# Performance work log

Measured on AMD Instinct MI355X. Metric: run time of the kernel, lower is better.

The kernel has to match this reference:

```python
import jax, jax.numpy as jnp
import numpy as np

N = 100000      # num nodes
E = 1600000     # num edges (avg degree 16)
IN = 128        # in_channels
OUT = 64        # out_channels
HID = 2 * OUT   # conv1 output width = 2*out_channels


def setup_inputs() -> dict:
    key = jax.random.key(0)
    k0, k1, k2, k3 = jax.random.split(key, 4)
    x = jax.random.uniform(k0, (N, IN), dtype=jnp.float32)
    edge_index = jax.random.randint(k1, (2, E), 0, N, dtype=jnp.int32)
    # GCNConv weights (glorot-style uniform), biases zero-init as in PyG
    s1 = float(np.sqrt(6.0 / (IN + HID)))
    W1 = jax.random.uniform(k2, (IN, HID), minval=-s1, maxval=s1, dtype=jnp.float32)
    b1 = jnp.zeros((HID,), dtype=jnp.float32)
    s2 = float(np.sqrt(6.0 / (HID + OUT)))
    W2 = jax.random.uniform(k3, (HID, OUT), minval=-s2, maxval=s2, dtype=jnp.float32)
    b2 = jnp.zeros((OUT,), dtype=jnp.float32)
    return {"x": x, "edge_index": edge_index, "W1": W1, "b1": b1, "W2": W2, "b2": b2}


def gcn_conv(x, W, b, src, dst, n):
    """PyG GCNConv: self-loops + symmetric deg^-1/2 normalization + scatter-add."""
    h = x @ W                                   # [n, d_out] dense transform first
    loops = jnp.arange(n, dtype=src.dtype)
    s = jnp.concatenate([src, loops])           # [E+n] sources (with self-loops)
    d = jnp.concatenate([dst, loops])           # [E+n] destinations
    deg = jax.ops.segment_sum(jnp.ones_like(s, dtype=h.dtype), d, num_segments=n)
    dinv = jnp.where(deg > 0, jax.lax.rsqrt(deg), 0.0)
    norm = dinv[s] * dinv[d]                    # [E+n]
    # gather -> scale -> scatter-add aggregation
    out = jax.ops.segment_sum(h[s] * norm[:, None], d, num_segments=n)
    return out + b


def reference(x, edge_index, W1, b1, W2, b2):
    src, dst = edge_index[0], edge_index[1]
    n = x.shape[0]
    h = jax.nn.relu(gcn_conv(x, W1, b1, src, dst, n))
    return gcn_conv(h, W2, b2, src, dst, n)
```

## Files before the change

### kernel.cpp

```cpp
#include <hip/hip_runtime.h>

#define IN_C  128
#define HID_C 128
#define OUT_C 64
#define NPB      128
#define NPB_SH   7
#define NPB_MASK 127
#define MAXB     2048
#define CAP      8192
#define B1_CHUNK 4096
#define PADQ     16
#define PADSLACK ((PADQ - 1) * NPB)

typedef __attribute__((ext_vector_type(8))) short short8;
typedef __attribute__((ext_vector_type(4))) float f32x4;

__device__ __forceinline__ unsigned short f2bf(float f) {
    unsigned u = __float_as_uint(f);
    unsigned r = (u + 0x7FFFu + ((u >> 16) & 1u)) >> 16;
    return (unsigned short)r;
}
__device__ __forceinline__ float bf_lo(unsigned u) { return __uint_as_float(u << 16); }
__device__ __forceinline__ float bf_hi(unsigned u) { return __uint_as_float(u & 0xFFFF0000u); }


__global__ __launch_bounds__(256) void hist_kernel(const int* __restrict__ dst,
                                                   int* __restrict__ bhist,
                                                   int E, int B) {
    __shared__ int lh[MAXB];
    int t = threadIdx.x;
    int e0 = blockIdx.x * B1_CHUNK;
    int nE = min(B1_CHUNK, E - e0);
    if (B <= MAXB) {
        for (int i = t; i < B; i += 256) lh[i] = 0;
        __syncthreads();
        for (int i = t; i < nE; i += 256) atomicAdd(&lh[dst[e0 + i] >> NPB_SH], 1);
        __syncthreads();
        for (int i = t; i < B; i += 256)
            if (lh[i]) atomicAdd(&bhist[i], lh[i]);
    } else {
        for (int i = t; i < nE; i += 256) atomicAdd(&bhist[dst[e0 + i] >> NPB_SH], 1);
    }
}

__global__ __launch_bounds__(1024) void scan_bucket_kernel(const int* __restrict__ bhist,
                                                           int* __restrict__ bbase,
                                                           int* __restrict__ bcur, int B) {
    __shared__ int sums[1024];
    int t = threadIdx.x;
    int chunk = (B + 1023) >> 10;
    int beg = t * chunk, end = min(beg + chunk, B);
    int s = 0;
    for (int i = beg; i < end; ++i) s += bhist[i];
    sums[t] = s;
    __syncthreads();
    for (int off = 1; off < 1024; off <<= 1) {
        int v = (t >= off) ? sums[t - off] : 0;
        __syncthreads();
        sums[t] += v;
        __syncthreads();
    }
    int run = (t == 0) ? 0 : sums[t - 1];
    for (int i = beg; i < end; ++i) {
        bbase[i] = run;
        bcur[i] = run + i * PADSLACK;
        run += bhist[i];
    }
    if (t == 1023) bbase[B] = sums[1023];
}

__global__ __launch_bounds__(256) void bucket_kernel(const int* __restrict__ src,
                                                     const int* __restrict__ dst,
                                                     int* __restrict__ bcur,
                                                     int* __restrict__ col,
                                                     int E, int B) {
    __shared__ int hist[MAXB];
    __shared__ int runb[MAXB];
    int t = threadIdx.x;
    int e0 = blockIdx.x * B1_CHUNK;
    int nE = min(B1_CHUNK, E - e0);
    if (B <= MAXB) {
        for (int i = t; i < B; i += 256) hist[i] = 0;
        __syncthreads();
        for (int i = t; i < nE; i += 256) atomicAdd(&hist[dst[e0 + i] >> NPB_SH], 1);
        __syncthreads();
        for (int i = t; i < B; i += 256) {
            int c = hist[i];
            runb[i] = c ? atomicAdd(&bcur[i], c) : 0;
            hist[i] = 0;
        }
        __syncthreads();
        for (int i = t; i < nE; i += 256) {
            int d = dst[e0 + i], s = src[e0 + i];
            int b = d >> NPB_SH;
            int off2 = atomicAdd(&hist[b], 1);
            col[runb[b] + off2] = (s << NPB_SH) | (d & NPB_MASK);
        }
    } else {
        for (int i = t; i < nE; i += 256) {
            int d = dst[e0 + i], s = src[e0 + i];
            int pos = atomicAdd(&bcur[d >> NPB_SH], 1);
            col[pos] = (s << NPB_SH) | (d & NPB_MASK);
        }
    }
}

__global__ __launch_bounds__(256) void csr_kernel(int* __restrict__ col,
                                                  const int* __restrict__ bbase,
                                                  int* __restrict__ rowptr,
                                                  int* __restrict__ rowend,
                                                  float* __restrict__ dinv,
                                                  int N, int E) {
    __shared__ int sorted[CAP];
    __shared__ int lhist[NPB];
    __shared__ int lpre[NPB + 1];
    int b = blockIdx.x;
    int t = threadIdx.x;
    int size = bbase[b + 1] - bbase[b];
    int pbase = bbase[b] + b * PADSLACK;
    int node_base = b << NPB_SH;
    int nn = min(NPB, N - node_base);

    if (t < NPB) lhist[t] = 0;
    __syncthreads();
    for (int i = t; i < size; i += 256) atomicAdd(&lhist[col[pbase + i] & NPB_MASK], 1);
    __syncthreads();
    if (t < NPB) lpre[t + 1] = (lhist[t] + PADQ - 1) & ~(PADQ - 1);
    if (t == 0) lpre[0] = 0;
    __syncthreads();
    for (int off = 1; off < NPB; off <<= 1) {
        int v = (t >= off && t < NPB) ? lpre[t + 1 - off] : 0;
        __syncthreads();
        if (t < NPB) lpre[t + 1] += v;
        __syncthreads();
    }
    if (t < nn) {
        rowptr[node_base + t] = pbase + lpre[t];
        rowend[node_base + t] = pbase + lpre[t + 1];
        dinv[node_base + t] = rsqrtf((float)(lhist[t] + 1));
    }
    if (t < NPB) lhist[t] = lpre[t];
    __syncthreads();
    int psize = lpre[NPB];
    if (psize <= CAP) {
        for (int i = t; i < psize; i += 256) sorted[i] = N;
        __syncthreads();
        for (int i = t; i < size; i += 256) {
            int entry = col[pbase + i];
            int slot = atomicAdd(&lhist[entry & NPB_MASK], 1);
            sorted[slot] = entry >> NPB_SH;
        }
        __syncthreads();
        for (int i = t; i < psize; i += 256) col[pbase + i] = sorted[i];
    } else {
        int ent[32];
        int c2 = 0;
        for (int i = t; i < size && c2 < 32; i += 256) ent[c2++] = col[pbase + i];
        __syncthreads();
        for (int i = t; i < psize; i += 256) col[pbase + i] = N;
        __syncthreads();
        c2 = 0;
        for (int i = t; i < size && c2 < 32; i += 256) {
            int entry = ent[c2++];
            int slot = atomicAdd(&lhist[entry & NPB_MASK], 1);
            col[pbase + slot] = entry >> NPB_SH;
        }
    }
}


template<int C, typename InT>
__global__ __launch_bounds__(256) void mm_mfma_kernel(
    const InT* __restrict__ X, const float* __restrict__ W,
    const float* __restrict__ dinv, unsigned short* __restrict__ Hs, int n) {
    constexpr int LD = 136;
    __shared__ unsigned short Wt[C][LD];
    int t = threadIdx.x;

    if (blockIdx.x == 0) {
        for (int i = t; i < C / 2; i += 256)
            ((unsigned*)(Hs + (size_t)n * C))[i] = 0;
    }

    for (int i = t; i < (128 * C) / 4; i += 256) {
        int idx = i * 4;
        int k = idx / C, c = idx % C;
        float4 wv = *(const float4*)&W[(size_t)k * C + c];
        Wt[c + 0][k] = f2bf(wv.x);
        Wt[c + 1][k] = f2bf(wv.y);
        Wt[c + 2][k] = f2bf(wv.z);
        Wt[c + 3][k] = f2bf(wv.w);
    }
    __syncthreads();

    int w = t >> 6, lane = t & 63;
    int m = lane & 15, quad = lane >> 4;
    int row0 = blockIdx.x * 64 + w * 16;
    int arow = min(row0 + m, n - 1);

    constexpr int NT = C / 16;
    f32x4 acc[NT];
#pragma unroll
    for (int ct = 0; ct < NT; ++ct) acc[ct] = (f32x4){0.f, 0.f, 0.f, 0.f};

#pragma unroll
    for (int kk = 0; kk < 4; ++kk) {
        int k0 = kk * 32 + quad * 8;
        short8 a;
        if constexpr (sizeof(InT) == 4) {
            const float* xp = (const float*)X + (size_t)arow * 128 + k0;
            float4 f0 = *(const float4*)xp;
            float4 f1 = *(const float4*)(xp + 4);
            a[0] = (short)f2bf(f0.x); a[1] = (short)f2bf(f0.y);
            a[2] = (short)f2bf(f0.z); a[3] = (short)f2bf(f0.w);
            a[4] = (short)f2bf(f1.x); a[5] = (short)f2bf(f1.y);
            a[6] = (short)f2bf(f1.z); a[7] = (short)f2bf(f1.w);
        } else {
            a = *(const short8*)((const unsigned short*)X + (size_t)arow * 128 + k0);
        }
#pragma unroll
        for (int ct = 0; ct < NT; ++ct) {
            short8 b = *(const short8*)&Wt[ct * 16 + m][k0];
            acc[ct] = __builtin_amdgcn_mfma_f32_16x16x32_bf16(a, b, acc[ct], 0, 0, 0);
        }
    }

    int qrow = row0 + quad * 4;
    float dv[4];
#pragma unroll
    for (int r = 0; r < 4; ++r) dv[r] = (qrow + r < n) ? dinv[qrow + r] : 0.f;
#pragma unroll
    for (int ct = 0; ct < NT; ++ct) {
        int c = ct * 16 + m;
#pragma unroll
        for (int r = 0; r < 4; ++r) {
            int row = qrow + r;
            if (row < n) Hs[(size_t)row * C + c] = f2bf(acc[ct][r] * dv[r]);
        }
    }
}


#define GBODY(NB)                                                              \
    {                                                                          \
        uint4 v[NB];                                                           \
        _Pragma("unroll") for (int b = 0; b < NB; ++b) {                       \
            int e = (g + b) * SLOTS + slot;                                    \
            int idx = __shfl(colv, e, 64);                                     \
            v[b] = *((const uint4*)(Hs + (size_t)idx * C) + cl);               \
        }                                                                      \
        _Pragma("unroll") for (int b = 0; b < NB; ++b) {                       \
            acc[0] += bf_lo(v[b].x); acc[1] += bf_hi(v[b].x);                  \
            acc[2] += bf_lo(v[b].y); acc[3] += bf_hi(v[b].y);                  \
            acc[4] += bf_lo(v[b].z); acc[5] += bf_hi(v[b].z);                  \
            acc[6] += bf_lo(v[b].w); acc[7] += bf_hi(v[b].w);                  \
        }                                                                      \
    }

template<int C, bool BOUT>
__global__ __launch_bounds__(256) void agg_kernel(
    const unsigned short* __restrict__ Hs, const float* __restrict__ bias,
    const float* __restrict__ dinv, const int* __restrict__ rowptr,
    const int* __restrict__ rowend, const int* __restrict__ col,
    void* __restrict__ outv, int n, int relu) {
    constexpr int LPR = C / 8;
    constexpr int SLOTS = 64 / LPR;
    int d = (blockIdx.x * 256 + threadIdx.x) >> 6;
    if (d >= n) return;
    int lane = threadIdx.x & 63;
    int cl = lane & (LPR - 1);
    int slot = lane / LPR;

    float acc[8] = {0.f, 0.f, 0.f, 0.f, 0.f, 0.f, 0.f, 0.f};
    int beg = rowptr[d], end = rowend[d];

    for (int j0 = beg; j0 < end; j0 += 64) {
        int cnt = min(64, end - j0);
        int colv = col[j0 + lane];
        int groups = cnt / SLOTS;
        int g = 0;
        for (; g + 4 <= groups; g += 4) GBODY(4)
        if constexpr (SLOTS == 8) {
            if (g < groups) GBODY(2)
        }
    }
#pragma unroll
    for (int mk = LPR; mk < 64; mk <<= 1) {
#pragma unroll
        for (int k = 0; k < 8; ++k) acc[k] += __shfl_xor(acc[k], mk, 64);
    }
    uint4 sv = *((const uint4*)(Hs + (size_t)d * C) + cl);
    acc[0] += bf_lo(sv.x); acc[1] += bf_hi(sv.x);
    acc[2] += bf_lo(sv.y); acc[3] += bf_hi(sv.y);
    acc[4] += bf_lo(sv.z); acc[5] += bf_hi(sv.z);
    acc[6] += bf_lo(sv.w); acc[7] += bf_hi(sv.w);

    float dv = dinv[d];
    float4 b0 = *((const float4*)bias + cl * 2);
    float4 b1 = *((const float4*)bias + cl * 2 + 1);
    float r[8];
    r[0] = dv * acc[0] + b0.x; r[1] = dv * acc[1] + b0.y;
    r[2] = dv * acc[2] + b0.z; r[3] = dv * acc[3] + b0.w;
    r[4] = dv * acc[4] + b1.x; r[5] = dv * acc[5] + b1.y;
    r[6] = dv * acc[6] + b1.z; r[7] = dv * acc[7] + b1.w;
    if (relu) {
#pragma unroll
        for (int k = 0; k < 8; ++k) r[k] = fmaxf(r[k], 0.f);
    }
    if (slot == 0) {
        if constexpr (BOUT) {
            uint4 o;
            o.x = (unsigned)f2bf(r[0]) | ((unsigned)f2bf(r[1]) << 16);
            o.y = (unsigned)f2bf(r[2]) | ((unsigned)f2bf(r[3]) << 16);
            o.z = (unsigned)f2bf(r[4]) | ((unsigned)f2bf(r[5]) << 16);
            o.w = (unsigned)f2bf(r[6]) | ((unsigned)f2bf(r[7]) << 16);
            *(uint4*)((unsigned short*)outv + (size_t)d * C + cl * 8) = o;
        } else {
            float* o = (float*)outv + (size_t)d * C + cl * 8;
            *(float4*)o = make_float4(r[0], r[1], r[2], r[3]);
            *(float4*)(o + 4) = make_float4(r[4], r[5], r[6], r[7]);
        }
    }
}


extern "C" void kernel_launch(void* const* d_in, const int* in_sizes, int n_in,
                              void* d_out, int out_size, void* d_ws, size_t ws_size,
                              hipStream_t stream) {
    const float* x  = (const float*)d_in[0];
    const int*   ei = (const int*)d_in[1];
    const float* W1 = (const float*)d_in[2];
    const float* b1 = (const float*)d_in[3];
    const float* W2 = (const float*)d_in[4];
    const float* b2 = (const float*)d_in[5];
    float* out = (float*)d_out;

    int N = in_sizes[0] / IN_C;
    int E = in_sizes[1] / 2;
    const int* src = ei;
    const int* dst = ei + E;
    int B = (N + NPB - 1) >> NPB_SH;
    int nblk = (E + B1_CHUNK - 1) / B1_CHUNK;

    char* ws = (char*)d_ws;
    size_t off = 0;
    int*   bhist  = (int*)(ws + off);   off += (size_t)B * 4;
    int*   bbase  = (int*)(ws + off);   off += (size_t)(B + 1) * 4;
    int*   bcur   = (int*)(ws + off);   off += (size_t)B * 4;
    float* dinv   = (float*)(ws + off); off += (size_t)N * 4;
    int*   rowptr = (int*)(ws + off);   off += (size_t)N * 4;
    int*   rowend = (int*)(ws + off);   off += (size_t)N * 4;
    off = (off + 15) & ~(size_t)15;
    int*   col    = (int*)(ws + off);   off += ((size_t)E + (size_t)B * PADSLACK + 64) * 4;
    off = (off + 15) & ~(size_t)15;
    unsigned short* H1  = (unsigned short*)(ws + off); off += (size_t)(N + 1) * HID_C * 2;
    off = (off + 15) & ~(size_t)15;
    unsigned short* AG1 = (unsigned short*)(ws + off); off += (size_t)N * HID_C * 2;
    unsigned short* H2 = H1;

    hipMemsetAsync(bhist, 0, (size_t)B * 4, stream);

    hist_kernel<<<nblk, 256, 0, stream>>>(dst, bhist, E, B);
    scan_bucket_kernel<<<1, 1024, 0, stream>>>(bhist, bbase, bcur, B);
    bucket_kernel<<<nblk, 256, 0, stream>>>(src, dst, bcur, col, E, B);
    csr_kernel<<<B, 256, 0, stream>>>(col, bbase, rowptr, rowend, dinv, N, E);

    int mblk = (N + 63) / 64;
    mm_mfma_kernel<HID_C, float><<<mblk, 256, 0, stream>>>(x, W1, dinv, H1, N);
    agg_kernel<HID_C, true><<<(N + 3) / 4, 256, 0, stream>>>(
        H1, b1, dinv, rowptr, rowend, col, AG1, N, 1);

    mm_mfma_kernel<OUT_C, unsigned short><<<mblk, 256, 0, stream>>>(AG1, W2, dinv, H2, N);
    agg_kernel<OUT_C, false><<<(N + 3) / 4, 256, 0, stream>>>(
        H2, b2, dinv, rowptr, rowend, col, out, N, 0);
}
```

Before: 347.3 us.

## Process multiple destination nodes per wavefront in aggregation kernels

The aggregation kernel now assigns NPN destination rows to each 64-lane wavefront (2 for the 128-wide layer, 4 for the 64-wide layer) and interleaves their neighbor gathers, so more independent loads are in flight per wave. Column indices are fetched with nontemporal loads. This aims to raise memory-level parallelism and amortize per-row setup, but costs more registers, idles lanes when neighboring rows have very different degrees, and launches fewer waves overall.

```diff
diff --git a/kernel.cpp b/kernel.cpp
--- a/kernel.cpp
+++ b/kernel.cpp
@@ -241,23 +241,7 @@
 }
 
 
-#define GBODY(NB)                                                              \
-    {                                                                          \
-        uint4 v[NB];                                                           \
-        _Pragma("unroll") for (int b = 0; b < NB; ++b) {                       \
-            int e = (g + b) * SLOTS + slot;                                    \
-            int idx = __shfl(colv, e, 64);                                     \
-            v[b] = *((const uint4*)(Hs + (size_t)idx * C) + cl);               \
-        }                                                                      \
-        _Pragma("unroll") for (int b = 0; b < NB; ++b) {                       \
-            acc[0] += bf_lo(v[b].x); acc[1] += bf_hi(v[b].x);                  \
-            acc[2] += bf_lo(v[b].y); acc[3] += bf_hi(v[b].y);                  \
-            acc[4] += bf_lo(v[b].z); acc[5] += bf_hi(v[b].z);                  \
-            acc[6] += bf_lo(v[b].w); acc[7] += bf_hi(v[b].w);                  \
-        }                                                                      \
-    }
-
-template<int C, bool BOUT>
+template<int C, bool BOUT, int NPN>
 __global__ __launch_bounds__(256) void agg_kernel(
     const unsigned short* __restrict__ Hs, const float* __restrict__ bias,
     const float* __restrict__ dinv, const int* __restrict__ rowptr,
@@ -265,60 +249,116 @@
     void* __restrict__ outv, int n, int relu) {
     constexpr int LPR = C / 8;
     constexpr int SLOTS = 64 / LPR;
-    int d = (blockIdx.x * 256 + threadIdx.x) >> 6;
-    if (d >= n) return;
+    constexpr int U = (SLOTS == 4) ? 4 : 2;
+    int wid = (blockIdx.x * 256 + threadIdx.x) >> 6;
+    int d0 = wid * NPN;
+    if (d0 >= n) return;
     int lane = threadIdx.x & 63;
     int cl = lane & (LPR - 1);
     int slot = lane / LPR;
 
-    float acc[8] = {0.f, 0.f, 0.f, 0.f, 0.f, 0.f, 0.f, 0.f};
-    int beg = rowptr[d], end = rowend[d];
-
-    for (int j0 = beg; j0 < end; j0 += 64) {
-        int cnt = min(64, end - j0);
-        int colv = col[j0 + lane];
-        int groups = cnt / SLOTS;
-        int g = 0;
-        for (; g + 4 <= groups; g += 4) GBODY(4)
-        if constexpr (SLOTS == 8) {
-            if (g < groups) GBODY(2)
-        }
-    }
-#pragma unroll
-    for (int mk = LPR; mk < 64; mk <<= 1) {
-#pragma unroll
-        for (int k = 0; k < 8; ++k) acc[k] += __shfl_xor(acc[k], mk, 64);
-    }
-    uint4 sv = *((const uint4*)(Hs + (size_t)d * C) + cl);
-    acc[0] += bf_lo(sv.x); acc[1] += bf_hi(sv.x);
-    acc[2] += bf_lo(sv.y); acc[3] += bf_hi(sv.y);
-    acc[4] += bf_lo(sv.z); acc[5] += bf_hi(sv.z);
-    acc[6] += bf_lo(sv.w); acc[7] += bf_hi(sv.w);
-
-    float dv = dinv[d];
+    int beg[NPN], len[NPN];
+    float dv[NPN];
+    uint4 sv[NPN];
+#pragma unroll
+    for (int k = 0; k < NPN; ++k) {
+        int d = d0 + k;
+        int dd = min(d, n - 1);
+        beg[k] = rowptr[dd];
+        len[k] = (d < n) ? (rowend[dd] - beg[k]) : 0;
+        dv[k] = dinv[dd];
+        sv[k] = *((const uint4*)(Hs + (size_t)dd * C) + cl);
+    }
+
+    float acc[NPN][8];
+#pragma unroll
+    for (int k = 0; k < NPN; ++k)
+#pragma unroll
+        for (int q = 0; q < 8; ++q) acc[k][q] = 0.f;
+
+    int lmax = 0;
+#pragma unroll
+    for (int k = 0; k < NPN; ++k) lmax = max(lmax, len[k]);
+
+    for (int j0 = 0; j0 < lmax; j0 += 64) {
+        int colv[NPN], groups[NPN];
+#pragma unroll
+        for (int k = 0; k < NPN; ++k)
+            colv[k] = __builtin_nontemporal_load(col + beg[k] + j0 + lane);
+#pragma unroll
+        for (int k = 0; k < NPN; ++k) {
+            int c = len[k] - j0;
+            c = c < 0 ? 0 : (c > 64 ? 64 : c);
+            groups[k] = c / SLOTS;
+        }
+        int gmax = 0;
+#pragma unroll
+        for (int k = 0; k < NPN; ++k) gmax = max(gmax, groups[k]);
+        for (int g = 0; g < gmax; g += U) {
+            uint4 v[NPN][U];
+#pragma unroll
+            for (int k = 0; k < NPN; ++k) {
+                if (g < groups[k]) {
+#pragma unroll
+                    for (int b = 0; b < U; ++b) {
+                        int e = (g + b) * SLOTS + slot;
+                        int idx = __shfl(colv[k], e, 64);
+                        v[k][b] = *((const uint4*)(Hs + (size_t)idx * C) + cl);
+                    }
+                }
+            }
+#pragma unroll
+            for (int k = 0; k < NPN; ++k) {
+                if (g < groups[k]) {
+#pragma unroll
+                    for (int b = 0; b < U; ++b) {
+                        acc[k][0] += bf_lo(v[k][b].x); acc[k][1] += bf_hi(v[k][b].x);
+                        acc[k][2] += bf_lo(v[k][b].y); acc[k][3] += bf_hi(v[k][b].y);
+                        acc[k][4] += bf_lo(v[k][b].z); acc[k][5] += bf_hi(v[k][b].z);
+                        acc[k][6] += bf_lo(v[k][b].w); acc[k][7] += bf_hi(v[k][b].w);
+                    }
+                }
+            }
+        }
+    }
+
     float4 b0 = *((const float4*)bias + cl * 2);
     float4 b1 = *((const float4*)bias + cl * 2 + 1);
-    float r[8];
-    r[0] = dv * acc[0] + b0.x; r[1] = dv * acc[1] + b0.y;
-    r[2] = dv * acc[2] + b0.z; r[3] = dv * acc[3] + b0.w;
-    r[4] = dv * acc[4] + b1.x; r[5] = dv * acc[5] + b1.y;
-    r[6] = dv * acc[6] + b1.z; r[7] = dv * acc[7] + b1.w;
-    if (relu) {
-#pragma unroll
-        for (int k = 0; k < 8; ++k) r[k] = fmaxf(r[k], 0.f);
-    }
-    if (slot == 0) {
-        if constexpr (BOUT) {
-            uint4 o;
-            o.x = (unsigned)f2bf(r[0]) | ((unsigned)f2bf(r[1]) << 16);
-            o.y = (unsigned)f2bf(r[2]) | ((unsigned)f2bf(r[3]) << 16);
-            o.z = (unsigned)f2bf(r[4]) | ((unsigned)f2bf(r[5]) << 16);
-            o.w = (unsigned)f2bf(r[6]) | ((unsigned)f2bf(r[7]) << 16);
-            *(uint4*)((unsigned short*)outv + (size_t)d * C + cl * 8) = o;
-        } else {
-            float* o = (float*)outv + (size_t)d * C + cl * 8;
-            *(float4*)o = make_float4(r[0], r[1], r[2], r[3]);
-            *(float4*)(o + 4) = make_float4(r[4], r[5], r[6], r[7]);
+#pragma unroll
+    for (int k = 0; k < NPN; ++k) {
+        int d = d0 + k;
+        if (d >= n) break;
+#pragma unroll
+        for (int mk = LPR; mk < 64; mk <<= 1) {
+#pragma unroll
+            for (int q = 0; q < 8; ++q) acc[k][q] += __shfl_xor(acc[k][q], mk, 64);
+        }
+        acc[k][0] += bf_lo(sv[k].x); acc[k][1] += bf_hi(sv[k].x);
+        acc[k][2] += bf_lo(sv[k].y); acc[k][3] += bf_hi(sv[k].y);
+        acc[k][4] += bf_lo(sv[k].z); acc[k][5] += bf_hi(sv[k].z);
+        acc[k][6] += bf_lo(sv[k].w); acc[k][7] += bf_hi(sv[k].w);
+        float r[8];
+        r[0] = dv[k] * acc[k][0] + b0.x; r[1] = dv[k] * acc[k][1] + b0.y;
+        r[2] = dv[k] * acc[k][2] + b0.z; r[3] = dv[k] * acc[k][3] + b0.w;
+        r[4] = dv[k] * acc[k][4] + b1.x; r[5] = dv[k] * acc[k][5] + b1.y;
+        r[6] = dv[k] * acc[k][6] + b1.z; r[7] = dv[k] * acc[k][7] + b1.w;
+        if (relu) {
+#pragma unroll
+            for (int q = 0; q < 8; ++q) r[q] = fmaxf(r[q], 0.f);
+        }
+        if (slot == 0) {
+            if constexpr (BOUT) {
+                uint4 o;
+                o.x = (unsigned)f2bf(r[0]) | ((unsigned)f2bf(r[1]) << 16);
+                o.y = (unsigned)f2bf(r[2]) | ((unsigned)f2bf(r[3]) << 16);
+                o.z = (unsigned)f2bf(r[4]) | ((unsigned)f2bf(r[5]) << 16);
+                o.w = (unsigned)f2bf(r[6]) | ((unsigned)f2bf(r[7]) << 16);
+                *(uint4*)((unsigned short*)outv + (size_t)d * C + cl * 8) = o;
+            } else {
+                float* o = (float*)outv + (size_t)d * C + cl * 8;
+                *(float4*)o = make_float4(r[0], r[1], r[2], r[3]);
+                *(float4*)(o + 4) = make_float4(r[4], r[5], r[6], r[7]);
+            }
         }
     }
 }
@@ -367,10 +407,10 @@
 
     int mblk = (N + 63) / 64;
     mm_mfma_kernel<HID_C, float><<<mblk, 256, 0, stream>>>(x, W1, dinv, H1, N);
-    agg_kernel<HID_C, true><<<(N + 3) / 4, 256, 0, stream>>>(
+    agg_kernel<HID_C, true, 2><<<(N + 7) / 8, 256, 0, stream>>>(
         H1, b1, dinv, rowptr, rowend, col, AG1, N, 1);
 
     mm_mfma_kernel<OUT_C, unsigned short><<<mblk, 256, 0, stream>>>(AG1, W2, dinv, H2, N);
-    agg_kernel<OUT_C, false><<<(N + 3) / 4, 256, 0, stream>>>(
+    agg_kernel<OUT_C, false, 4><<<(N + 15) / 16, 256, 0, stream>>>(
         H2, b2, dinv, rowptr, rowend, col, out, N, 0);
 }
```

Result: slower. 357.3 us (+2.9%).

## Stage bucketed edges in LDS for coalesced writes; preconvert weights to bf16 once

Applied to the files above, without the earlier changes.

The bucket kernel now does a block-local prefix scan over bucket counts and first sorts the chunk's edges into shared memory. It then writes them out in bucket-contiguous runs, replacing scattered per-edge global writes with mostly contiguous ones. Separately, the weight transpose and bf16 conversion moves into a small pre-pass kernel, so each matmul block only copies the prepared weights with vector loads. This adds two tiny launches, more LDS use per bucket block (which may lower occupancy), and extra scan synchronisation.

```diff
diff --git a/kernel.cpp b/kernel.cpp
--- a/kernel.cpp
+++ b/kernel.cpp
@@ -75,7 +75,11 @@
                                                      int* __restrict__ col,
                                                      int E, int B) {
     __shared__ int hist[MAXB];
-    __shared__ int runb[MAXB];
+    __shared__ int lbase[MAXB];
+    __shared__ int gbase[MAXB];
+    __shared__ int part[256];
+    __shared__ int stage[B1_CHUNK];
+    __shared__ short bstage[B1_CHUNK];
     int t = threadIdx.x;
     int e0 = blockIdx.x * B1_CHUNK;
     int nE = min(B1_CHUNK, E - e0);
@@ -84,17 +88,39 @@
         __syncthreads();
         for (int i = t; i < nE; i += 256) atomicAdd(&hist[dst[e0 + i] >> NPB_SH], 1);
         __syncthreads();
-        for (int i = t; i < B; i += 256) {
+        int chunk = (B + 255) >> 8;
+        int beg = t * chunk, end = min(beg + chunk, B);
+        int s = 0;
+        for (int i = beg; i < end; ++i) s += hist[i];
+        part[t] = s;
+        __syncthreads();
+        for (int off = 1; off < 256; off <<= 1) {
+            int v = (t >= off) ? part[t - off] : 0;
+            __syncthreads();
+            part[t] += v;
+            __syncthreads();
+        }
+        int run = (t == 0) ? 0 : part[t - 1];
+        for (int i = beg; i < end; ++i) {
             int c = hist[i];
-            runb[i] = c ? atomicAdd(&bcur[i], c) : 0;
-            hist[i] = 0;
-        }
+            lbase[i] = run;
+            gbase[i] = c ? atomicAdd(&bcur[i], c) : 0;
+            run += c;
+        }
+        __syncthreads();
+        for (int i = t; i < B; i += 256) hist[i] = lbase[i];
         __syncthreads();
         for (int i = t; i < nE; i += 256) {
-            int d = dst[e0 + i], s = src[e0 + i];
+            int d = dst[e0 + i], s2 = src[e0 + i];
             int b = d >> NPB_SH;
-            int off2 = atomicAdd(&hist[b], 1);
-            col[runb[b] + off2] = (s << NPB_SH) | (d & NPB_MASK);
+            int slot = atomicAdd(&hist[b], 1);
+            stage[slot] = (s2 << NPB_SH) | (d & NPB_MASK);
+            bstage[slot] = (short)b;
+        }
+        __syncthreads();
+        for (int i = t; i < nE; i += 256) {
+            int b = bstage[i];
+            col[gbase[b] + (i - lbase[b])] = stage[i];
         }
     } else {
         for (int i = t; i < nE; i += 256) {
@@ -168,10 +194,24 @@
     }
 }
 
+__global__ __launch_bounds__(256) void wcvt_kernel(const float* __restrict__ W,
+                                                   unsigned short* __restrict__ Wt,
+                                                   int C) {
+    int i = blockIdx.x * 256 + threadIdx.x;
+    if (i >= 32 * C) return;
+    int idx = i * 4;
+    int k = idx / C, c = idx % C;
+    float4 wv = *(const float4*)&W[(size_t)k * C + c];
+    Wt[(size_t)(c + 0) * 128 + k] = f2bf(wv.x);
+    Wt[(size_t)(c + 1) * 128 + k] = f2bf(wv.y);
+    Wt[(size_t)(c + 2) * 128 + k] = f2bf(wv.z);
+    Wt[(size_t)(c + 3) * 128 + k] = f2bf(wv.w);
+}
+
 
 template<int C, typename InT>
 __global__ __launch_bounds__(256) void mm_mfma_kernel(
-    const InT* __restrict__ X, const float* __restrict__ W,
+    const InT* __restrict__ X, const unsigned short* __restrict__ Wpre,
     const float* __restrict__ dinv, unsigned short* __restrict__ Hs, int n) {
     constexpr int LD = 136;
     __shared__ unsigned short Wt[C][LD];
@@ -182,14 +222,10 @@
             ((unsigned*)(Hs + (size_t)n * C))[i] = 0;
     }
 
-    for (int i = t; i < (128 * C) / 4; i += 256) {
-        int idx = i * 4;
-        int k = idx / C, c = idx % C;
-        float4 wv = *(const float4*)&W[(size_t)k * C + c];
-        Wt[c + 0][k] = f2bf(wv.x);
-        Wt[c + 1][k] = f2bf(wv.y);
-        Wt[c + 2][k] = f2bf(wv.z);
-        Wt[c + 3][k] = f2bf(wv.w);
+    for (int i = t; i < (C * 128) / 8; i += 256) {
+        int idx = i * 8;
+        int c = idx >> 7, k = idx & 127;
+        *(short8*)&Wt[c][k] = *(const short8*)&Wpre[idx];
     }
     __syncthreads();
 
@@ -356,9 +392,15 @@
     unsigned short* H1  = (unsigned short*)(ws + off); off += (size_t)(N + 1) * HID_C * 2;
     off = (off + 15) & ~(size_t)15;
     unsigned short* AG1 = (unsigned short*)(ws + off); off += (size_t)N * HID_C * 2;
+    off = (off + 15) & ~(size_t)15;
+    unsigned short* Wt1 = (unsigned short*)(ws + off); off += (size_t)128 * 128 * 2;
+    unsigned short* Wt2 = (unsigned short*)(ws + off); off += (size_t)128 * 64 * 2;
     unsigned short* H2 = H1;
 
     hipMemsetAsync(bhist, 0, (size_t)B * 4, stream);
+
+    wcvt_kernel<<<16, 256, 0, stream>>>(W1, Wt1, HID_C);
+    wcvt_kernel<<<8, 256, 0, stream>>>(W2, Wt2, OUT_C);
 
     hist_kernel<<<nblk, 256, 0, stream>>>(dst, bhist, E, B);
     scan_bucket_kernel<<<1, 1024, 0, stream>>>(bhist, bbase, bcur, B);
@@ -366,11 +408,11 @@
     csr_kernel<<<B, 256, 0, stream>>>(col, bbase, rowptr, rowend, dinv, N, E);
 
     int mblk = (N + 63) / 64;
-    mm_mfma_kernel<HID_C, float><<<mblk, 256, 0, stream>>>(x, W1, dinv, H1, N);
+    mm_mfma_kernel<HID_C, float><<<mblk, 256, 0, stream>>>(x, Wt1, dinv, H1, N);
     agg_kernel<HID_C, true><<<(N + 3) / 4, 256, 0, stream>>>(
         H1, b1, dinv, rowptr, rowend, col, AG1, N, 1);
 
-    mm_mfma_kernel<OUT_C, unsigned short><<<mblk, 256, 0, stream>>>(AG1, W2, dinv, H2, N);
+    mm_mfma_kernel<OUT_C, unsigned short><<<mblk, 256, 0, stream>>>(AG1, Wt2, dinv, H2, N);
     agg_kernel<OUT_C, false><<<(N + 3) / 4, 256, 0, stream>>>(
         H2, b2, dinv, rowptr, rowend, col, out, N, 0);
 }
```

After: 342.8 us. No clear change (-1.3%).
